# Optimization experiments

Hardware: AMD Instinct MI355X
Metric: run time of the kernel (lower is better)

Reference implementation:

```python
import jax, jax.numpy as jnp
import numpy as np

M = 1024      # mol_dim
H = 1024      # ffn_hidden
T = 2048      # sequence length
NS = 5        # n_solvents
DE = 64       # desc_emb_dim
NB = 3        # ffn/residual blocks
HIN = 2 * M + DE + 1  # beta head input dim


def setup_inputs() -> dict:
    key = jax.random.key(0)
    ks = jax.random.split(key, 32)
    w = lambda i, shape: (0.02 * jax.random.normal(ks[i], shape, dtype=jnp.float32))
    inp = {
        "mol_vec": jax.random.normal(ks[0], (M,), dtype=jnp.float32),
        "solvent_seq": jax.random.uniform(ks[1], (T, NS), dtype=jnp.float32),
        "desc_seq": jax.random.normal(ks[2], (T, 6), dtype=jnp.float32),
        "solvent_vecs": jax.random.normal(ks[3], (NS, M), dtype=jnp.float32),
        "boundary_mask": jnp.zeros((T,), dtype=bool),
        # SolventProjection: Linear(5*M -> M) + 3 residual FFN blocks
        "sp_proj_w": w(4, (NS * M, M)), "sp_proj_b": jnp.zeros((M,), jnp.float32),
        "sp_fc1_w": w(5, (NB, M, M)), "sp_fc1_b": jnp.zeros((NB, M), jnp.float32),
        "sp_fc2_w": w(6, (NB, M, M)), "sp_fc2_b": jnp.zeros((NB, M), jnp.float32),
        "sp_ln_g": jnp.ones((NB, M), jnp.float32), "sp_ln_b": jnp.zeros((NB, M), jnp.float32),
        # desc_proj: Linear(6 -> 64)
        "desc_w": w(7, (6, DE)), "desc_b": jnp.zeros((DE,), jnp.float32),
        "bh_proj_w": w(8, (HIN, H)), "bh_proj_b": jnp.zeros((H,), jnp.float32),
        "bh_fc1_w": w(9, (NB, H, H)), "bh_fc1_b": jnp.zeros((NB, H), jnp.float32),
        "bh_fc2_w": w(10, (NB, H, H)), "bh_fc2_b": jnp.zeros((NB, H), jnp.float32),
        "bh_ln_g": jnp.ones((NB, H), jnp.float32), "bh_ln_b": jnp.zeros((NB, H), jnp.float32),
        "mu_w": w(11, (H,)), "mu_b": jnp.zeros((1,), jnp.float32),
        "phi_w": w(12, (H,)), "phi_b": jnp.zeros((1,), jnp.float32),
    }
    return inp


def _gelu(x):
    return jax.nn.gelu(x, approximate=False)  # torch nn.GELU default (erf)


def _ln(x, g, b, eps=1e-5):
    m = jnp.mean(x, axis=-1, keepdims=True)
    v = jnp.mean((x - m) ** 2, axis=-1, keepdims=True)
    return g * (x - m) * jax.lax.rsqrt(v + eps) + b


def _res_blocks(x, w1, b1, w2, b2, g, b):
    # stack of ResidualFFNBlock (dropout=0 / eval mode)
    for i in range(w1.shape[0]):
        x = _ln(_gelu(x @ w1[i] + b1[i]) @ w2[i] + b2[i] + x, g[i], b[i])
    return x


def reference(mol_vec, solvent_seq, desc_seq, solvent_vecs, boundary_mask,
              sp_proj_w, sp_proj_b, sp_fc1_w, sp_fc1_b, sp_fc2_w, sp_fc2_b, sp_ln_g, sp_ln_b,
              desc_w, desc_b,
              bh_proj_w, bh_proj_b, bh_fc1_w, bh_fc1_b, bh_fc2_w, bh_fc2_b, bh_ln_g, bh_ln_b,
              mu_w, mu_b, phi_w, phi_b):
    def step(prev_rf, xs):
        ratios, desc, is_b = xs  # [5], [6], scalar bool
        # SolventProjection: scale each solvent vec by its ratio, concat, project
        sv = (solvent_vecs * ratios[:, None]).reshape(-1)         # [5*M]
        sp = _gelu(sv @ sp_proj_w + sp_proj_b)                     # [M]
        sp = _res_blocks(sp, sp_fc1_w, sp_fc1_b, sp_fc2_w, sp_fc2_b, sp_ln_g, sp_ln_b)
        demb = _gelu(desc @ desc_w + desc_b)                       # [DE]
        x = jnp.concatenate([mol_vec, sp, demb, prev_rf[None]])   # [HIN]
        z = _gelu(x @ bh_proj_w + bh_proj_b)                       # [H]
        z = _res_blocks(z, bh_fc1_w, bh_fc1_b, bh_fc2_w, bh_fc2_b, bh_ln_g, bh_ln_b)
        mu = jax.nn.sigmoid(jnp.dot(z, mu_w) + mu_b[0])
        phi = jax.nn.softplus(jnp.dot(z, phi_w) + phi_b[0]) + 2.0
        # monotonic update: restart at system boundaries or before first prediction
        rf = jnp.where(is_b | (prev_rf < 0), mu, prev_rf + mu * (1.0 - prev_rf))
        return jax.lax.stop_gradient(rf), (rf, mu, phi)  # prev_rf is detached in torch

    prev0 = jnp.float32(-1.0)
    _, (rfs, mus, phis) = jax.lax.scan(step, prev0, (solvent_seq, desc_seq, boundary_mask))
    return jnp.stack([rfs, mus, phis])  # [3, T]
```

## Files before the change

### kernel.cpp

```cpp
#include <hip/hip_runtime.h>
#include <math.h>

#define MDIM 1024
#define TSEQ 2048
#define NSOL 5
#define DED  64
#define NBLK 3
#define KITER 3
#define XLDB 1088
#define NRED 6144
#define RST  64

typedef __bf16 bf16x8 __attribute__((ext_vector_type(8)));
typedef __bf16 bf16x4 __attribute__((ext_vector_type(4)));
typedef float  f32x4  __attribute__((ext_vector_type(4)));

#define GLDS16(gptr, lptr) __builtin_amdgcn_global_load_lds( \
    (const __attribute__((address_space(1))) unsigned int*)(const void*)(gptr), \
    (__attribute__((address_space(3))) unsigned int*)(void*)(lptr), 16, 0, 0)

__device__ __forceinline__ float gelu_f(float x){
  return 0.5f * x * (1.0f + erff(x * 0.70710678118654752440f));
}
__device__ __forceinline__ float sigmoid_f(float x){ return 1.0f/(1.0f+expf(-x)); }
__device__ __forceinline__ float softplus_f(float x){ return fmaxf(x,0.0f) + log1pf(expf(-fabsf(x))); }

__global__ __launch_bounds__(256) void k_cvtT13(const float* __restrict__ s0,
    const float* __restrict__ s1, const float* __restrict__ s2, const float* __restrict__ s3,
    const float* __restrict__ s4, __bf16* __restrict__ dst, __bf16* __restrict__ WpT){
  __shared__ float t[32][33];
  const size_t MM = (size_t)MDIM*MDIM;
  int z = blockIdx.z;
  int tx = threadIdx.x & 31, ty = threadIdx.x >> 5;
  if (z < 12){
    if (blockIdx.y >= 32) return;
    const float* s = (z<3)? s0 + (size_t)z*MM : (z<6)? s1 + (size_t)(z-3)*MM :
                     (z<9)? s2 + (size_t)(z-6)*MM : s3 + (size_t)(z-9)*MM;
    __bf16* d = dst + (size_t)z*MM;
    int k0 = blockIdx.y*32, n0 = blockIdx.x*32;
    #pragma unroll
    for (int r=0;r<32;r+=8) t[ty+r][tx] = s[(size_t)(k0+ty+r)*MDIM + n0+tx];
    __syncthreads();
    #pragma unroll
    for (int r=0;r<32;r+=8) d[(size_t)(n0+ty+r)*MDIM + k0+tx] = (__bf16)t[tx][ty+r];
  } else {
    int k0 = blockIdx.y*32, n0 = blockIdx.x*32;
    #pragma unroll
    for (int r=0;r<32;r+=8) t[ty+r][tx] = s4[(size_t)(k0+ty+r)*MDIM + n0+tx];
    __syncthreads();
    #pragma unroll
    for (int r=0;r<32;r+=8) WpT[(size_t)(n0+ty+r)*XLDB + k0+tx] = (__bf16)t[tx][ty+r];
  }
}

__global__ __launch_bounds__(256) void k_pm(const float* __restrict__ sv,
    const float* __restrict__ spW, const float* __restrict__ mol,
    const float* __restrict__ bhw, float* __restrict__ PART){
  int s = blockIdx.y;
  int j = blockIdx.x*256 + threadIdx.x;
  int z = blockIdx.z, k0 = z*64;
  if (s < NSOL){
    const float* w = spW + (size_t)s*MDIM*MDIM + (size_t)k0*MDIM + j;
    const float* v = sv + s*MDIM + k0;
    float acc = 0.f;
    for (int k=0;k<64;k++) acc = fmaf(v[k], w[(size_t)k*MDIM], acc);
    PART[(size_t)z*NRED + s*MDIM + j] = acc;
  } else {
    const float* w = bhw + (size_t)k0*MDIM + j;
    float acc = 0.f;
    for (int k=0;k<64;k++) acc = fmaf(mol[k0+k], w[(size_t)k*MDIM], acc);
    PART[(size_t)z*NRED + 5120 + j] = acc;
  }
}

__global__ __launch_bounds__(256) void k_red(const float* __restrict__ PART,
    const float* __restrict__ bhb, float* __restrict__ P, float* __restrict__ mp,
    float* __restrict__ prevg, int* __restrict__ dlist, int* __restrict__ dcnt){
  int i = blockIdx.x*256 + threadIdx.x;
  if (i < TSEQ){ prevg[i] = (i==0)? -1.0f : 1.0f; dlist[i] = i; }
  if (i == 0) *dcnt = TSEQ;
  float a = 0.f;
  #pragma unroll
  for (int z=0;z<16;z++) a += PART[(size_t)z*NRED + i];
  if (i < 5120) P[i] = a;
  else mp[i-5120] = a + bhb[i-5120];
}

__global__ __launch_bounds__(256) void k_sp0d(const float* __restrict__ ratios,
    const float* __restrict__ P, const float* __restrict__ bias,
    const float* __restrict__ desc, const float* __restrict__ dw,
    const float* __restrict__ db,
    float* __restrict__ X, __bf16* __restrict__ Xb){
  int t = blockIdx.y;
  if (blockIdx.x < 4){
    int j = blockIdx.x*256 + threadIdx.x;
    const float* r = ratios + t*NSOL;
    float acc = bias[j];
    #pragma unroll
    for (int s=0;s<NSOL;s++) acc = fmaf(r[s], P[s*MDIM+j], acc);
    float v = gelu_f(acc);
    X[(size_t)t*MDIM + j] = v;
    Xb[(size_t)t*XLDB + j] = (__bf16)v;
  } else if (threadIdx.x < DED){
    int e = threadIdx.x;
    const float* d = desc + t*6;
    float acc = db[e];
    #pragma unroll
    for (int c=0;c<6;c++) acc = fmaf(d[c], dw[c*DED+e], acc);
    Xb[(size_t)t*XLDB + MDIM + e] = (__bf16)gelu_f(acc);
  }
}

template<int BK, bool GELU, bool RES, bool OUTF, bool OUTB, bool Z0>
__global__ __launch_bounds__(512) void k_mfma_gemm(
    const __bf16* __restrict__ A, int lda, int K,
    const __bf16* __restrict__ Bt,
    const float* __restrict__ bias,
    const float* __restrict__ R, int ldr,
    float* __restrict__ Cf, int ldcf,
    __bf16* __restrict__ Cb, int ldcb,
    const float* __restrict__ wlast, const float* __restrict__ prevg,
    float* __restrict__ Z0f, __bf16* __restrict__ Z0b)
{
  constexpr int CPR = BK/8;
  constexpr int AG  = BK/32;
  constexpr int BG  = (BK>=64)? BK/64 : 1;
  constexpr int KS  = BK/32;
  __shared__ __attribute__((aligned(16))) __bf16 As[2][128*BK];
  __shared__ __attribute__((aligned(16))) __bf16 Bs[2][64*BK];
  int tid = threadIdx.x;
  int wave = tid>>6, lane = tid&63;
  int row0 = blockIdx.y*128, col0 = blockIdx.x*64;
  int wr = (wave>>1)*32, wc = (wave&1)*32;
  int lr = lane&15;
  f32x4 acc[2][2] = {};
  int NT = K / BK;

  auto stage = [&](int b, int k0){
    #pragma unroll
    for (int p=0;p<AG;p++){
      int q = wave*(AG*64) + p*64 + lane;
      int r = q/CPR, c = q%CPR, cl = c^(r&7);
      GLDS16(A + (size_t)(row0+r)*lda + k0 + cl*8, &As[b][(wave*(AG*64)+p*64)*8]);
    }
    #pragma unroll
    for (int p=0;p<BG;p++){
      int q = wave*(BG*64) + p*64 + lane;
      int r = q/CPR, c = q%CPR, cl = c^(r&7);
      GLDS16(Bt + (size_t)(col0+r)*K + k0 + cl*8, &Bs[b][(wave*(BG*64)+p*64)*8]);
    }
  };

  stage(0, 0);
  for (int t=0; t<NT; t++){
    __syncthreads();
    if (t+1 < NT) stage((t+1)&1, (t+1)*BK);
    int b = t&1;
    #pragma unroll
    for (int ks=0;ks<KS;ks++){
      int c = ks*4 + (lane>>4);
      bf16x8 af[2], bg[2];
      #pragma unroll
      for (int m=0;m<2;m++){
        int rowA = wr + m*16 + lr;
        af[m] = *(const bf16x8*)&As[b][rowA*BK + ((c ^ (rowA&7))<<3)];
      }
      #pragma unroll
      for (int n=0;n<2;n++){
        int rowB = wc + n*16 + lr;
        bg[n] = *(const bf16x8*)&Bs[b][rowB*BK + ((c ^ (rowB&7))<<3)];
      }
      #pragma unroll
      for (int m=0;m<2;m++)
        #pragma unroll
        for (int n=0;n<2;n++)
          acc[m][n] = __builtin_amdgcn_mfma_f32_16x16x32_bf16(af[m], bg[n], acc[m][n], 0,0,0);
    }
  }
  int rq = (lane>>4)*4;
  #pragma unroll
  for (int m=0;m<2;m++){
    #pragma unroll
    for (int n=0;n<2;n++){
      int cc = col0 + wc + n*16 + lr;
      float bv = bias[cc];
      #pragma unroll
      for (int q=0;q<4;q++){
        int r = row0 + wr + m*16 + rq + q;
        float v = acc[m][n][q] + bv;
        if (RES)  v += R[(size_t)r*ldr + cc];
        if (GELU) v = gelu_f(v);
        if (OUTF) Cf[(size_t)r*ldcf + cc] = v;
        if (OUTB) Cb[(size_t)r*ldcb + cc] = (__bf16)v;
        if (Z0){
          float z = gelu_f(v + prevg[r]*wlast[cc]);
          Z0f[(size_t)r*MDIM + cc] = z;
          Z0b[(size_t)r*MDIM + cc] = (__bf16)z;
        }
      }
    }
  }
}

template<bool MUPHI>
__global__ __launch_bounds__(256) void k_ln(const float* __restrict__ Y, int ldy,
    float* __restrict__ Xo, int ldx, __bf16* __restrict__ Xb, int ldxb,
    const float* __restrict__ g, const float* __restrict__ b,
    const float* __restrict__ muw, const float* __restrict__ mub,
    const float* __restrict__ phiw, const float* __restrict__ phib,
    float* __restrict__ muA, float* __restrict__ phiA)
{
  int t = blockIdx.x;
  __shared__ float red[16];
  int tid = threadIdx.x;
  f32x4 y = *(const f32x4*)&Y[(size_t)t*ldy + tid*4];
  float s  = y[0]+y[1]+y[2]+y[3];
  float s2 = y[0]*y[0]+y[1]*y[1]+y[2]*y[2]+y[3]*y[3];
  for (int o=32;o>0;o>>=1){ s += __shfl_down(s,o); s2 += __shfl_down(s2,o); }
  int wid = tid>>6, lane = tid&63;
  if (lane==0){ red[wid]=s; red[wid+8]=s2; }
  __syncthreads();
  if (tid==0){
    float a=0.f,c=0.f;
    for (int w=0;w<4;w++){ a+=red[w]; c+=red[w+8]; }
    red[0]=a; red[8]=c;
  }
  __syncthreads();
  float mean = red[0]*(1.0f/MDIM);
  float var  = red[8]*(1.0f/MDIM) - mean*mean;
  float rs = rsqrtf(var + 1e-5f);
  f32x4 gv = *(const f32x4*)&g[tid*4];
  f32x4 bb = *(const f32x4*)&b[tid*4];
  f32x4 v; bf16x4 vb;
  #pragma unroll
  for (int i=0;i<4;i++){ v[i] = gv[i]*(y[i]-mean)*rs + bb[i]; vb[i] = (__bf16)v[i]; }
  *(f32x4*)&Xo[(size_t)t*ldx + tid*4] = v;
  *(bf16x4*)&Xb[(size_t)t*ldxb + tid*4] = vb;
  if (MUPHI){
    f32x4 mw = *(const f32x4*)&muw[tid*4];
    f32x4 pw = *(const f32x4*)&phiw[tid*4];
    float sm=0.f, sp=0.f;
    #pragma unroll
    for (int i=0;i<4;i++){ sm = fmaf(v[i], mw[i], sm); sp = fmaf(v[i], pw[i], sp); }
    for (int o=32;o>0;o>>=1){ sm+=__shfl_down(sm,o); sp+=__shfl_down(sp,o); }
    __syncthreads();
    if (lane==0){ red[wid]=sm; red[wid+8]=sp; }
    __syncthreads();
    if (tid==0){
      float a=0.f,c=0.f;
      for (int w=0;w<4;w++){ a+=red[w]; c+=red[w+8]; }
      muA[t]  = sigmoid_f(a + mub[0]);
      phiA[t] = softplus_f(c + phib[0]) + 2.0f;
    }
  }
}


__global__ __launch_bounds__(256) void k_fc1z_dirty(
    const float* __restrict__ ZP, const float* __restrict__ wlast,
    const float* __restrict__ prevg,
    const __bf16* __restrict__ Wt, const float* __restrict__ bias,
    const int* __restrict__ dlist, const int* __restrict__ dcnt,
    float* __restrict__ Z, __bf16* __restrict__ Zb, __bf16* __restrict__ Ob)
{
  __shared__ __bf16 zl[MDIM];
  int nd = *dcnt;
  int jb = blockIdx.x;
  int j = jb*256 + threadIdx.x;
  for (int rs = blockIdx.y; rs < nd; rs += RST){
    int t = dlist[rs];
    float prev = prevg[t];
    #pragma unroll
    for (int q=0;q<4;q++){
      int k = threadIdx.x + 256*q;
      float v = gelu_f(ZP[(size_t)t*MDIM + k] + prev*wlast[k]);
      zl[k] = (__bf16)v;
      if (jb==0){ Z[(size_t)t*MDIM + k] = v; Zb[(size_t)t*MDIM + k] = (__bf16)v; }
    }
    __syncthreads();
    const __bf16* w = Wt + (size_t)j*MDIM;
    float acc = 0.f;
    for (int k=0;k<MDIM;k+=8){
      bf16x8 wv = *(const bf16x8*)&w[k];
      bf16x8 iv = *(const bf16x8*)&zl[k];
      #pragma unroll
      for (int u=0;u<8;u++) acc = fmaf((float)wv[u], (float)iv[u], acc);
    }
    acc = gelu_f(acc + bias[j]);
    Ob[(size_t)t*MDIM + j] = (__bf16)acc;
    __syncthreads();
  }
}

__global__ __launch_bounds__(256) void k_fc2_dirty(
    const __bf16* __restrict__ In, const __bf16* __restrict__ Wt,
    const float* __restrict__ bias, const float* __restrict__ Rz,
    const int* __restrict__ dlist, const int* __restrict__ dcnt,
    float* __restrict__ Of)
{
  int nd = *dcnt;
  int j = blockIdx.x*256 + threadIdx.x;
  for (int rs = blockIdx.y; rs < nd; rs += RST){
    int t = dlist[rs];
    const __bf16* in = In + (size_t)t*MDIM;
    const __bf16* w  = Wt + (size_t)j*MDIM;
    float acc = 0.f;
    for (int k=0;k<MDIM;k+=8){
      bf16x8 wv = *(const bf16x8*)&w[k];
      bf16x8 iv = *(const bf16x8*)&in[k];
      #pragma unroll
      for (int u=0;u<8;u++) acc = fmaf((float)wv[u], (float)iv[u], acc);
    }
    Of[(size_t)t*MDIM + j] = acc + bias[j] + Rz[(size_t)t*MDIM + j];
  }
}

__global__ __launch_bounds__(256) void k_lnfc1_dirty(
    const float* __restrict__ Y,
    const float* __restrict__ g, const float* __restrict__ b,
    const __bf16* __restrict__ Wt, const float* __restrict__ fbias,
    const int* __restrict__ dlist, const int* __restrict__ dcnt,
    float* __restrict__ Z, __bf16* __restrict__ Zb, __bf16* __restrict__ Ob)
{
  __shared__ __bf16 zl[MDIM];
  __shared__ float red[16];
  int nd = *dcnt;
  int jb = blockIdx.x;
  int j = jb*256 + threadIdx.x;
  int wid = threadIdx.x>>6, lane = threadIdx.x&63;
  for (int rs = blockIdx.y; rs < nd; rs += RST){
    int t = dlist[rs];
    float y[4]; float s=0.f, s2=0.f;
    #pragma unroll
    for (int q=0;q<4;q++){
      y[q] = Y[(size_t)t*MDIM + threadIdx.x + 256*q];
      s += y[q]; s2 += y[q]*y[q];
    }
    for (int o=32;o>0;o>>=1){ s += __shfl_down(s,o); s2 += __shfl_down(s2,o); }
    if (lane==0){ red[wid]=s; red[wid+8]=s2; }
    __syncthreads();
    if (threadIdx.x==0){
      float a=0.f,c=0.f;
      for (int w=0;w<4;w++){ a+=red[w]; c+=red[w+8]; }
      red[0]=a; red[8]=c;
    }
    __syncthreads();
    float mean = red[0]*(1.0f/MDIM);
    float var  = red[8]*(1.0f/MDIM) - mean*mean;
    float rs2 = rsqrtf(var + 1e-5f);
    #pragma unroll
    for (int q=0;q<4;q++){
      int k = threadIdx.x + 256*q;
      float v = g[k]*(y[q]-mean)*rs2 + b[k];
      zl[k] = (__bf16)v;
      if (jb==0){ Z[(size_t)t*MDIM + k] = v; Zb[(size_t)t*MDIM + k] = (__bf16)v; }
    }
    __syncthreads();
    const __bf16* w = Wt + (size_t)j*MDIM;
    float acc = 0.f;
    for (int k=0;k<MDIM;k+=8){
      bf16x8 wv = *(const bf16x8*)&w[k];
      bf16x8 iv = *(const bf16x8*)&zl[k];
      #pragma unroll
      for (int u=0;u<8;u++) acc = fmaf((float)wv[u], (float)iv[u], acc);
    }
    acc = gelu_f(acc + fbias[j]);
    Ob[(size_t)t*MDIM + j] = (__bf16)acc;
    __syncthreads();
  }
}

__global__ __launch_bounds__(256) void k_lnmp_dirty(
    const float* __restrict__ Y,
    const float* __restrict__ g, const float* __restrict__ b,
    const int* __restrict__ dlist, const int* __restrict__ dcnt,
    const float* __restrict__ muw, const float* __restrict__ mub,
    const float* __restrict__ phiw, const float* __restrict__ phib,
    float* __restrict__ muA, float* __restrict__ phiA)
{
  int nd = *dcnt;
  __shared__ float red[16];
  int wid = threadIdx.x>>6, lane = threadIdx.x&63;
  for (int rs = blockIdx.x; rs < nd; rs += RST){
    int t = dlist[rs];
    float y[4]; float s=0.f, s2=0.f;
    #pragma unroll
    for (int q=0;q<4;q++){
      y[q] = Y[(size_t)t*MDIM + threadIdx.x + 256*q];
      s += y[q]; s2 += y[q]*y[q];
    }
    for (int o=32;o>0;o>>=1){ s += __shfl_down(s,o); s2 += __shfl_down(s2,o); }
    if (lane==0){ red[wid]=s; red[wid+8]=s2; }
    __syncthreads();
    if (threadIdx.x==0){
      float a=0.f,c=0.f;
      for (int w=0;w<4;w++){ a+=red[w]; c+=red[w+8]; }
      red[0]=a; red[8]=c;
    }
    __syncthreads();
    float mean = red[0]*(1.0f/MDIM);
    float var  = red[8]*(1.0f/MDIM) - mean*mean;
    float rs2 = rsqrtf(var + 1e-5f);
    float sm=0.f, sp=0.f;
    #pragma unroll
    for (int q=0;q<4;q++){
      int k = threadIdx.x + 256*q;
      float v = g[k]*(y[q]-mean)*rs2 + b[k];
      sm = fmaf(v, muw[k], sm); sp = fmaf(v, phiw[k], sp);
    }
    __syncthreads();
    for (int o=32;o>0;o>>=1){ sm+=__shfl_down(sm,o); sp+=__shfl_down(sp,o); }
    if (lane==0){ red[wid]=sm; red[wid+8]=sp; }
    __syncthreads();
    if (threadIdx.x==0){
      float a=0.f,c=0.f;
      for (int w=0;w<4;w++){ a+=red[w]; c+=red[w+8]; }
      muA[t]  = sigmoid_f(a + mub[0]);
      phiA[t] = softplus_f(c + phib[0]) + 2.0f;
    }
    __syncthreads();
  }
}

__global__ __launch_bounds__(1024) void k_scan(
    const float* __restrict__ muA, const float* __restrict__ phiA,
    const unsigned char* __restrict__ bmask,
    float* __restrict__ prevg, int* __restrict__ dlist, int* __restrict__ dcnt,
    float* __restrict__ out)
{
  if (*dcnt == 0) return;
  __shared__ float v[2][TSEQ];
  __shared__ unsigned char f[2][TSEQ];
  __shared__ int cnt;
  int tid = threadIdx.x;
  if (tid==0) cnt = 0;
  for (int i=tid;i<TSEQ;i+=1024){
    v[0][i] = 1.0f - muA[i];
    f[0][i] = (i==0) || (bmask[i] != 0);
  }
  __syncthreads();
  int src=0;
  for (int off=1; off<TSEQ; off<<=1){
    int dst = src^1;
    for (int i=tid;i<TSEQ;i+=1024){
      float vv = v[src][i]; unsigned char ff = f[src][i];
      if (i>=off && !ff){ vv *= v[src][i-off]; ff = f[src][i-off]; }
      v[dst][i]=vv; f[dst][i]=ff;
    }
    __syncthreads();
    src = dst;
  }
  for (int i=tid;i<TSEQ;i+=1024){
    float rf = 1.0f - v[src][i];
    float prev = (i==0) ? -1.0f : (1.0f - v[src][i-1]);
    out[i]        = rf;
    out[TSEQ+i]   = muA[i];
    out[2*TSEQ+i] = phiA[i];
    float old = prevg[i];
    prevg[i] = prev;
    if (fabsf(prev - old) > 1e-3f){
      int pos = atomicAdd(&cnt, 1);
      dlist[pos] = i;
    }
  }
  __syncthreads();
  if (tid==0) *dcnt = cnt;
}

extern "C" void kernel_launch(void* const* d_in, const int* in_sizes, int n_in,
                              void* d_out, int out_size, void* d_ws, size_t ws_size,
                              hipStream_t stream) {
  const float* mol       = (const float*)d_in[0];
  const float* ratios    = (const float*)d_in[1];
  const float* desc      = (const float*)d_in[2];
  const float* svvec     = (const float*)d_in[3];
  const unsigned char* bmask = (const unsigned char*)d_in[4];
  const float* sp_proj_w = (const float*)d_in[5];
  const float* sp_proj_b = (const float*)d_in[6];
  const float* sp_fc1_w  = (const float*)d_in[7];
  const float* sp_fc1_b  = (const float*)d_in[8];
  const float* sp_fc2_w  = (const float*)d_in[9];
  const float* sp_fc2_b  = (const float*)d_in[10];
  const float* sp_ln_g   = (const float*)d_in[11];
  const float* sp_ln_b   = (const float*)d_in[12];
  const float* desc_w    = (const float*)d_in[13];
  const float* desc_b    = (const float*)d_in[14];
  const float* bh_proj_w = (const float*)d_in[15];
  const float* bh_proj_b = (const float*)d_in[16];
  const float* bh_fc1_w  = (const float*)d_in[17];
  const float* bh_fc1_b  = (const float*)d_in[18];
  const float* bh_fc2_w  = (const float*)d_in[19];
  const float* bh_fc2_b  = (const float*)d_in[20];
  const float* bh_ln_g   = (const float*)d_in[21];
  const float* bh_ln_b   = (const float*)d_in[22];
  const float* mu_w      = (const float*)d_in[23];
  const float* mu_b      = (const float*)d_in[24];
  const float* phi_w     = (const float*)d_in[25];
  const float* phi_b     = (const float*)d_in[26];
  float* out = (float*)d_out;

  char* p = (char*)d_ws;
  auto alloc = [&](size_t bytes)->char*{ char* r = p; p += (bytes + 255) & ~(size_t)255; return r; };
  const size_t MM = (size_t)MDIM*MDIM;
  float*  X    = (float*)alloc((size_t)TSEQ*MDIM*4);
  __bf16* Xb   = (__bf16*)alloc((size_t)TSEQ*XLDB*2);
  __bf16* Zb   = (__bf16*)alloc((size_t)TSEQ*MDIM*2);
  float*  Y    = (float*)alloc((size_t)TSEQ*MDIM*4);
  float*  ZP   = (float*)alloc((size_t)TSEQ*MDIM*4);
  __bf16* Hb16 = (__bf16*)alloc((size_t)TSEQ*MDIM*2);
  __bf16* WALL = (__bf16*)alloc(12*MM*2);
  __bf16* WpT  = (__bf16*)alloc((size_t)MDIM*XLDB*2);
  float*  PART = (float*)alloc((size_t)16*NRED*4);
  float*  P    = (float*)alloc((size_t)NSOL*MDIM*4);
  float*  mp   = (float*)alloc(MDIM*4);
  float*  prevg= (float*)alloc(TSEQ*4);
  float*  muA  = (float*)alloc(TSEQ*4);
  float*  phiA = (float*)alloc(TSEQ*4);
  int*    dlist= (int*)alloc(TSEQ*4);
  int*    dcnt = (int*)alloc(256);
  __bf16* W1T = WALL, *W2T = WALL + 3*MM, *U1T = WALL + 6*MM, *U2T = WALL + 9*MM;
  float*  Z    = X;

  k_cvtT13<<<dim3(32,34,13),256,0,stream>>>(sp_fc1_w, sp_fc2_w, bh_fc1_w, bh_fc2_w,
      bh_proj_w + MM, WALL, WpT);
  k_pm<<<dim3(4,6,16),256,0,stream>>>(svvec, sp_proj_w, mol, bh_proj_w, PART);
  k_red<<<dim3(NRED/256),256,0,stream>>>(PART, bh_proj_b, P, mp, prevg, dlist, dcnt);
  k_sp0d<<<dim3(5,TSEQ),256,0,stream>>>(ratios, P, sp_proj_b, desc, desc_w, desc_b, X, Xb);

  const float* wlast = bh_proj_w + (size_t)2112*MDIM;
  for (int i=0;i<NBLK;i++){
    k_mfma_gemm<128,true,false,false,true,false><<<dim3(16,16),512,0,stream>>>(
        Xb, XLDB, MDIM, W1T + i*MM, sp_fc1_b + i*MDIM, nullptr, 0,
        nullptr, 0, Hb16, MDIM, nullptr, nullptr, nullptr, nullptr);
    k_mfma_gemm<128,false,true,true,false,false><<<dim3(16,16),512,0,stream>>>(
        Hb16, MDIM, MDIM, W2T + i*MM, sp_fc2_b + i*MDIM, X, MDIM,
        Y, MDIM, nullptr, 0, nullptr, nullptr, nullptr, nullptr);
    k_ln<false><<<dim3(TSEQ),256,0,stream>>>(Y, MDIM, X, MDIM, Xb, XLDB,
        sp_ln_g + i*MDIM, sp_ln_b + i*MDIM,
        nullptr, nullptr, nullptr, nullptr, nullptr, nullptr);
  }
  k_mfma_gemm<64,false,false,true,false,true><<<dim3(16,16),512,0,stream>>>(
      Xb, XLDB, XLDB, WpT, mp, nullptr, 0, ZP, MDIM, nullptr, 0,
      wlast, prevg, Z, Zb);

  for (int i=0;i<NBLK;i++){
    k_mfma_gemm<128,true,false,false,true,false><<<dim3(16,16),512,0,stream>>>(
        Zb, MDIM, MDIM, U1T + i*MM, bh_fc1_b + i*MDIM, nullptr, 0,
        nullptr, 0, Hb16, MDIM, nullptr, nullptr, nullptr, nullptr);
    k_mfma_gemm<128,false,true,true,false,false><<<dim3(16,16),512,0,stream>>>(
        Hb16, MDIM, MDIM, U2T + i*MM, bh_fc2_b + i*MDIM, Z, MDIM,
        Y, MDIM, nullptr, 0, nullptr, nullptr, nullptr, nullptr);
    if (i < NBLK-1)
      k_ln<false><<<dim3(TSEQ),256,0,stream>>>(Y, MDIM, Z, MDIM, Zb, MDIM,
          bh_ln_g + i*MDIM, bh_ln_b + i*MDIM,
          nullptr, nullptr, nullptr, nullptr, nullptr, nullptr);
    else
      k_ln<true><<<dim3(TSEQ),256,0,stream>>>(Y, MDIM, Z, MDIM, Zb, MDIM,
          bh_ln_g + i*MDIM, bh_ln_b + i*MDIM,
          mu_w, mu_b, phi_w, phi_b, muA, phiA);
  }
  k_scan<<<dim3(1),1024,0,stream>>>(muA, phiA, bmask, prevg, dlist, dcnt, out);

  for (int it=1; it<KITER; it++){
    k_fc1z_dirty<<<dim3(4,RST),256,0,stream>>>(ZP, wlast, prevg,
        U1T, bh_fc1_b, dlist, dcnt, Z, Zb, Hb16);
    k_fc2_dirty<<<dim3(4,RST),256,0,stream>>>(
        Hb16, U2T, bh_fc2_b, Z, dlist, dcnt, Y);
    for (int i=1;i<NBLK;i++){
      k_lnfc1_dirty<<<dim3(4,RST),256,0,stream>>>(Y,
          bh_ln_g + (i-1)*MDIM, bh_ln_b + (i-1)*MDIM,
          U1T + i*MM, bh_fc1_b + i*MDIM, dlist, dcnt, Z, Zb, Hb16);
      k_fc2_dirty<<<dim3(4,RST),256,0,stream>>>(
          Hb16, U2T + i*MM, bh_fc2_b + i*MDIM, Z, dlist, dcnt, Y);
    }
    k_lnmp_dirty<<<dim3(RST),256,0,stream>>>(Y,
        bh_ln_g + (NBLK-1)*MDIM, bh_ln_b + (NBLK-1)*MDIM,
        dlist, dcnt, mu_w, mu_b, phi_w, phi_b, muA, phiA);
    k_scan<<<dim3(1),1024,0,stream>>>(muA, phiA, bmask, prevg, dlist, dcnt, out);
  }
  (void)in_sizes; (void)n_in; (void)out_size; (void)ws_size;
}
```

Measured before the change: 414.7 us.

## Drop fp32 residual copies and shrink dirty kernels to single-wave blocks

```diff
diff --git a/kernel.cpp b/kernel.cpp
--- a/kernel.cpp
+++ b/kernel.cpp
@@ -89,8 +89,7 @@
 __global__ __launch_bounds__(256) void k_sp0d(const float* __restrict__ ratios,
     const float* __restrict__ P, const float* __restrict__ bias,
     const float* __restrict__ desc, const float* __restrict__ dw,
-    const float* __restrict__ db,
-    float* __restrict__ X, __bf16* __restrict__ Xb){
+    const float* __restrict__ db, __bf16* __restrict__ Xb){
   int t = blockIdx.y;
   if (blockIdx.x < 4){
     int j = blockIdx.x*256 + threadIdx.x;
@@ -98,9 +97,7 @@
     float acc = bias[j];
     #pragma unroll
     for (int s=0;s<NSOL;s++) acc = fmaf(r[s], P[s*MDIM+j], acc);
-    float v = gelu_f(acc);
-    X[(size_t)t*MDIM + j] = v;
-    Xb[(size_t)t*XLDB + j] = (__bf16)v;
+    Xb[(size_t)t*XLDB + j] = (__bf16)gelu_f(acc);
   } else if (threadIdx.x < DED){
     int e = threadIdx.x;
     const float* d = desc + t*6;
@@ -116,11 +113,11 @@
     const __bf16* __restrict__ A, int lda, int K,
     const __bf16* __restrict__ Bt,
     const float* __restrict__ bias,
-    const float* __restrict__ R, int ldr,
+    const __bf16* __restrict__ R, int ldr,
     float* __restrict__ Cf, int ldcf,
     __bf16* __restrict__ Cb, int ldcb,
     const float* __restrict__ wlast, const float* __restrict__ prevg,
-    float* __restrict__ Z0f, __bf16* __restrict__ Z0b)
+    __bf16* __restrict__ Z0b)
 {
   constexpr int CPR = BK/8;
   constexpr int AG  = BK/32;
@@ -188,15 +185,11 @@
       for (int q=0;q<4;q++){
         int r = row0 + wr + m*16 + rq + q;
         float v = acc[m][n][q] + bv;
-        if (RES)  v += R[(size_t)r*ldr + cc];
+        if (RES)  v += (float)R[(size_t)r*ldr + cc];
         if (GELU) v = gelu_f(v);
         if (OUTF) Cf[(size_t)r*ldcf + cc] = v;
         if (OUTB) Cb[(size_t)r*ldcb + cc] = (__bf16)v;
-        if (Z0){
-          float z = gelu_f(v + prevg[r]*wlast[cc]);
-          Z0f[(size_t)r*MDIM + cc] = z;
-          Z0b[(size_t)r*MDIM + cc] = (__bf16)z;
-        }
+        if (Z0)   Z0b[(size_t)r*MDIM + cc] = (__bf16)gelu_f(v + prevg[r]*wlast[cc]);
       }
     }
   }
@@ -204,7 +197,7 @@
 
 template<bool MUPHI>
 __global__ __launch_bounds__(256) void k_ln(const float* __restrict__ Y, int ldy,
-    float* __restrict__ Xo, int ldx, __bf16* __restrict__ Xb, int ldxb,
+    __bf16* __restrict__ Xb, int ldxb,
     const float* __restrict__ g, const float* __restrict__ b,
     const float* __restrict__ muw, const float* __restrict__ mub,
     const float* __restrict__ phiw, const float* __restrict__ phib,
@@ -234,7 +227,6 @@
   f32x4 v; bf16x4 vb;
   #pragma unroll
   for (int i=0;i<4;i++){ v[i] = gv[i]*(y[i]-mean)*rs + bb[i]; vb[i] = (__bf16)v[i]; }
-  *(f32x4*)&Xo[(size_t)t*ldx + tid*4] = v;
   *(bf16x4*)&Xb[(size_t)t*ldxb + tid*4] = vb;
   if (MUPHI){
     f32x4 mw = *(const f32x4*)&muw[tid*4];
@@ -256,26 +248,26 @@
 }
 
 
-__global__ __launch_bounds__(256) void k_fc1z_dirty(
+__global__ __launch_bounds__(64) void k_fc1z_dirty(
     const float* __restrict__ ZP, const float* __restrict__ wlast,
     const float* __restrict__ prevg,
     const __bf16* __restrict__ Wt, const float* __restrict__ bias,
     const int* __restrict__ dlist, const int* __restrict__ dcnt,
-    float* __restrict__ Z, __bf16* __restrict__ Zb, __bf16* __restrict__ Ob)
+    __bf16* __restrict__ Zb, __bf16* __restrict__ Ob)
 {
   __shared__ __bf16 zl[MDIM];
   int nd = *dcnt;
   int jb = blockIdx.x;
-  int j = jb*256 + threadIdx.x;
+  int j = jb*64 + threadIdx.x;
   for (int rs = blockIdx.y; rs < nd; rs += RST){
     int t = dlist[rs];
     float prev = prevg[t];
     #pragma unroll
-    for (int q=0;q<4;q++){
-      int k = threadIdx.x + 256*q;
-      float v = gelu_f(ZP[(size_t)t*MDIM + k] + prev*wlast[k]);
-      zl[k] = (__bf16)v;
-      if (jb==0){ Z[(size_t)t*MDIM + k] = v; Zb[(size_t)t*MDIM + k] = (__bf16)v; }
+    for (int q=0;q<16;q++){
+      int k = threadIdx.x + 64*q;
+      __bf16 v = (__bf16)gelu_f(ZP[(size_t)t*MDIM + k] + prev*wlast[k]);
+      zl[k] = v;
+      if (jb==0) Zb[(size_t)t*MDIM + k] = v;
     }
     __syncthreads();
     const __bf16* w = Wt + (size_t)j*MDIM;
@@ -286,20 +278,19 @@
       #pragma unroll
       for (int u=0;u<8;u++) acc = fmaf((float)wv[u], (float)iv[u], acc);
     }
-    acc = gelu_f(acc + bias[j]);
-    Ob[(size_t)t*MDIM + j] = (__bf16)acc;
-    __syncthreads();
-  }
-}
-
-__global__ __launch_bounds__(256) void k_fc2_dirty(
+    Ob[(size_t)t*MDIM + j] = (__bf16)gelu_f(acc + bias[j]);
+    __syncthreads();
+  }
+}
+
+__global__ __launch_bounds__(64) void k_fc2_dirty(
     const __bf16* __restrict__ In, const __bf16* __restrict__ Wt,
-    const float* __restrict__ bias, const float* __restrict__ Rz,
+    const float* __restrict__ bias, const __bf16* __restrict__ Rz,
     const int* __restrict__ dlist, const int* __restrict__ dcnt,
     float* __restrict__ Of)
 {
   int nd = *dcnt;
-  int j = blockIdx.x*256 + threadIdx.x;
+  int j = blockIdx.x*64 + threadIdx.x;
   for (int rs = blockIdx.y; rs < nd; rs += RST){
     int t = dlist[rs];
     const __bf16* in = In + (size_t)t*MDIM;
@@ -311,49 +302,41 @@
       #pragma unroll
       for (int u=0;u<8;u++) acc = fmaf((float)wv[u], (float)iv[u], acc);
     }
-    Of[(size_t)t*MDIM + j] = acc + bias[j] + Rz[(size_t)t*MDIM + j];
-  }
-}
-
-__global__ __launch_bounds__(256) void k_lnfc1_dirty(
+    Of[(size_t)t*MDIM + j] = acc + bias[j] + (float)Rz[(size_t)t*MDIM + j];
+  }
+}
+
+__global__ __launch_bounds__(64) void k_lnfc1_dirty(
     const float* __restrict__ Y,
     const float* __restrict__ g, const float* __restrict__ b,
     const __bf16* __restrict__ Wt, const float* __restrict__ fbias,
     const int* __restrict__ dlist, const int* __restrict__ dcnt,
-    float* __restrict__ Z, __bf16* __restrict__ Zb, __bf16* __restrict__ Ob)
+    __bf16* __restrict__ Zb, __bf16* __restrict__ Ob)
 {
   __shared__ __bf16 zl[MDIM];
-  __shared__ float red[16];
   int nd = *dcnt;
   int jb = blockIdx.x;
-  int j = jb*256 + threadIdx.x;
-  int wid = threadIdx.x>>6, lane = threadIdx.x&63;
+  int j = jb*64 + threadIdx.x;
   for (int rs = blockIdx.y; rs < nd; rs += RST){
     int t = dlist[rs];
-    float y[4]; float s=0.f, s2=0.f;
-    #pragma unroll
-    for (int q=0;q<4;q++){
-      y[q] = Y[(size_t)t*MDIM + threadIdx.x + 256*q];
+    float y[16]; float s=0.f, s2=0.f;
+    #pragma unroll
+    for (int q=0;q<16;q++){
+      y[q] = Y[(size_t)t*MDIM + threadIdx.x + 64*q];
       s += y[q]; s2 += y[q]*y[q];
     }
     for (int o=32;o>0;o>>=1){ s += __shfl_down(s,o); s2 += __shfl_down(s2,o); }
-    if (lane==0){ red[wid]=s; red[wid+8]=s2; }
-    __syncthreads();
-    if (threadIdx.x==0){
-      float a=0.f,c=0.f;
-      for (int w=0;w<4;w++){ a+=red[w]; c+=red[w+8]; }
-      red[0]=a; red[8]=c;
-    }
-    __syncthreads();
-    float mean = red[0]*(1.0f/MDIM);
-    float var  = red[8]*(1.0f/MDIM) - mean*mean;
+    float tot  = __shfl(s, 0);
+    float tot2 = __shfl(s2, 0);
+    float mean = tot*(1.0f/MDIM);
+    float var  = tot2*(1.0f/MDIM) - mean*mean;
     float rs2 = rsqrtf(var + 1e-5f);
     #pragma unroll
-    for (int q=0;q<4;q++){
-      int k = threadIdx.x + 256*q;
-      float v = g[k]*(y[q]-mean)*rs2 + b[k];
-      zl[k] = (__bf16)v;
-      if (jb==0){ Z[(size_t)t*MDIM + k] = v; Zb[(size_t)t*MDIM + k] = (__bf16)v; }
+    for (int q=0;q<16;q++){
+      int k = threadIdx.x + 64*q;
+      __bf16 v = (__bf16)(g[k]*(y[q]-mean)*rs2 + b[k]);
+      zl[k] = v;
+      if (jb==0) Zb[(size_t)t*MDIM + k] = v;
     }
     __syncthreads();
     const __bf16* w = Wt + (size_t)j*MDIM;
@@ -364,13 +347,12 @@
       #pragma unroll
       for (int u=0;u<8;u++) acc = fmaf((float)wv[u], (float)iv[u], acc);
     }
-    acc = gelu_f(acc + fbias[j]);
-    Ob[(size_t)t*MDIM + j] = (__bf16)acc;
-    __syncthreads();
-  }
-}
-
-__global__ __launch_bounds__(256) void k_lnmp_dirty(
+    Ob[(size_t)t*MDIM + j] = (__bf16)gelu_f(acc + fbias[j]);
+    __syncthreads();
+  }
+}
+
+__global__ __launch_bounds__(64) void k_lnmp_dirty(
     const float* __restrict__ Y,
     const float* __restrict__ g, const float* __restrict__ b,
     const int* __restrict__ dlist, const int* __restrict__ dcnt,
@@ -379,46 +361,32 @@
     float* __restrict__ muA, float* __restrict__ phiA)
 {
   int nd = *dcnt;
-  __shared__ float red[16];
-  int wid = threadIdx.x>>6, lane = threadIdx.x&63;
   for (int rs = blockIdx.x; rs < nd; rs += RST){
     int t = dlist[rs];
-    float y[4]; float s=0.f, s2=0.f;
-    #pragma unroll
-    for (int q=0;q<4;q++){
-      y[q] = Y[(size_t)t*MDIM + threadIdx.x + 256*q];
+    float y[16]; float s=0.f, s2=0.f;
+    #pragma unroll
+    for (int q=0;q<16;q++){
+      y[q] = Y[(size_t)t*MDIM + threadIdx.x + 64*q];
       s += y[q]; s2 += y[q]*y[q];
     }
     for (int o=32;o>0;o>>=1){ s += __shfl_down(s,o); s2 += __shfl_down(s2,o); }
-    if (lane==0){ red[wid]=s; red[wid+8]=s2; }
-    __syncthreads();
-    if (threadIdx.x==0){
-      float a=0.f,c=0.f;
-      for (int w=0;w<4;w++){ a+=red[w]; c+=red[w+8]; }
-      red[0]=a; red[8]=c;
-    }
-    __syncthreads();
-    float mean = red[0]*(1.0f/MDIM);
-    float var  = red[8]*(1.0f/MDIM) - mean*mean;
+    float tot  = __shfl(s, 0);
+    float tot2 = __shfl(s2, 0);
+    float mean = tot*(1.0f/MDIM);
+    float var  = tot2*(1.0f/MDIM) - mean*mean;
     float rs2 = rsqrtf(var + 1e-5f);
     float sm=0.f, sp=0.f;
     #pragma unroll
-    for (int q=0;q<4;q++){
-      int k = threadIdx.x + 256*q;
+    for (int q=0;q<16;q++){
+      int k = threadIdx.x + 64*q;
       float v = g[k]*(y[q]-mean)*rs2 + b[k];
       sm = fmaf(v, muw[k], sm); sp = fmaf(v, phiw[k], sp);
     }
-    __syncthreads();
     for (int o=32;o>0;o>>=1){ sm+=__shfl_down(sm,o); sp+=__shfl_down(sp,o); }
-    if (lane==0){ red[wid]=sm; red[wid+8]=sp; }
-    __syncthreads();
     if (threadIdx.x==0){
-      float a=0.f,c=0.f;
-      for (int w=0;w<4;w++){ a+=red[w]; c+=red[w+8]; }
-      muA[t]  = sigmoid_f(a + mub[0]);
-      phiA[t] = softplus_f(c + phib[0]) + 2.0f;
-    }
-    __syncthreads();
+      muA[t]  = sigmoid_f(sm + mub[0]);
+      phiA[t] = softplus_f(sp + phib[0]) + 2.0f;
+    }
   }
 }
 
@@ -502,7 +470,6 @@
   char* p = (char*)d_ws;
   auto alloc = [&](size_t bytes)->char*{ char* r = p; p += (bytes + 255) & ~(size_t)255; return r; };
   const size_t MM = (size_t)MDIM*MDIM;
-  float*  X    = (float*)alloc((size_t)TSEQ*MDIM*4);
   __bf16* Xb   = (__bf16*)alloc((size_t)TSEQ*XLDB*2);
   __bf16* Zb   = (__bf16*)alloc((size_t)TSEQ*MDIM*2);
   float*  Y    = (float*)alloc((size_t)TSEQ*MDIM*4);
@@ -519,61 +486,60 @@
   int*    dlist= (int*)alloc(TSEQ*4);
   int*    dcnt = (int*)alloc(256);
   __bf16* W1T = WALL, *W2T = WALL + 3*MM, *U1T = WALL + 6*MM, *U2T = WALL + 9*MM;
-  float*  Z    = X;
 
   k_cvtT13<<<dim3(32,34,13),256,0,stream>>>(sp_fc1_w, sp_fc2_w, bh_fc1_w, bh_fc2_w,
       bh_proj_w + MM, WALL, WpT);
   k_pm<<<dim3(4,6,16),256,0,stream>>>(svvec, sp_proj_w, mol, bh_proj_w, PART);
   k_red<<<dim3(NRED/256),256,0,stream>>>(PART, bh_proj_b, P, mp, prevg, dlist, dcnt);
-  k_sp0d<<<dim3(5,TSEQ),256,0,stream>>>(ratios, P, sp_proj_b, desc, desc_w, desc_b, X, Xb);
+  k_sp0d<<<dim3(5,TSEQ),256,0,stream>>>(ratios, P, sp_proj_b, desc, desc_w, desc_b, Xb);
 
   const float* wlast = bh_proj_w + (size_t)2112*MDIM;
   for (int i=0;i<NBLK;i++){
     k_mfma_gemm<128,true,false,false,true,false><<<dim3(16,16),512,0,stream>>>(
         Xb, XLDB, MDIM, W1T + i*MM, sp_fc1_b + i*MDIM, nullptr, 0,
-        nullptr, 0, Hb16, MDIM, nullptr, nullptr, nullptr, nullptr);
+        nullptr, 0, Hb16, MDIM, nullptr, nullptr, nullptr);
     k_mfma_gemm<128,false,true,true,false,false><<<dim3(16,16),512,0,stream>>>(
-        Hb16, MDIM, MDIM, W2T + i*MM, sp_fc2_b + i*MDIM, X, MDIM,
-        Y, MDIM, nullptr, 0, nullptr, nullptr, nullptr, nullptr);
-    k_ln<false><<<dim3(TSEQ),256,0,stream>>>(Y, MDIM, X, MDIM, Xb, XLDB,
+        Hb16, MDIM, MDIM, W2T + i*MM, sp_fc2_b + i*MDIM, Xb, XLDB,
+        Y, MDIM, nullptr, 0, nullptr, nullptr, nullptr);
+    k_ln<false><<<dim3(TSEQ),256,0,stream>>>(Y, MDIM, Xb, XLDB,
         sp_ln_g + i*MDIM, sp_ln_b + i*MDIM,
         nullptr, nullptr, nullptr, nullptr, nullptr, nullptr);
   }
   k_mfma_gemm<64,false,false,true,false,true><<<dim3(16,16),512,0,stream>>>(
       Xb, XLDB, XLDB, WpT, mp, nullptr, 0, ZP, MDIM, nullptr, 0,
-      wlast, prevg, Z, Zb);
+      wlast, prevg, Zb);
 
   for (int i=0;i<NBLK;i++){
     k_mfma_gemm<128,true,false,false,true,false><<<dim3(16,16),512,0,stream>>>(
         Zb, MDIM, MDIM, U1T + i*MM, bh_fc1_b + i*MDIM, nullptr, 0,
-        nullptr, 0, Hb16, MDIM, nullptr, nullptr, nullptr, nullptr);
+        nullptr, 0, Hb16, MDIM, nullptr, nullptr, nullptr);
     k_mfma_gemm<128,false,true,true,false,false><<<dim3(16,16),512,0,stream>>>(
-        Hb16, MDIM, MDIM, U2T + i*MM, bh_fc2_b + i*MDIM, Z, MDIM,
-        Y, MDIM, nullptr, 0, nullptr, nullptr, nullptr, nullptr);
+        Hb16, MDIM, MDIM, U2T + i*MM, bh_fc2_b + i*MDIM, Zb, MDIM,
+        Y, MDIM, nullptr, 0, nullptr, nullptr, nullptr);
     if (i < NBLK-1)
-      k_ln<false><<<dim3(TSEQ),256,0,stream>>>(Y, MDIM, Z, MDIM, Zb, MDIM,
+      k_ln<false><<<dim3(TSEQ),256,0,stream>>>(Y, MDIM, Zb, MDIM,
           bh_ln_g + i*MDIM, bh_ln_b + i*MDIM,
           nullptr, nullptr, nullptr, nullptr, nullptr, nullptr);
     else
-      k_ln<true><<<dim3(TSEQ),256,0,stream>>>(Y, MDIM, Z, MDIM, Zb, MDIM,
+      k_ln<true><<<dim3(TSEQ),256,0,stream>>>(Y, MDIM, Zb, MDIM,
           bh_ln_g + i*MDIM, bh_ln_b + i*MDIM,
           mu_w, mu_b, phi_w, phi_b, muA, phiA);
   }
   k_scan<<<dim3(1),1024,0,stream>>>(muA, phiA, bmask, prevg, dlist, dcnt, out);
 
   for (int it=1; it<KITER; it++){
-    k_fc1z_dirty<<<dim3(4,RST),256,0,stream>>>(ZP, wlast, prevg,
-        U1T, bh_fc1_b, dlist, dcnt, Z, Zb, Hb16);
-    k_fc2_dirty<<<dim3(4,RST),256,0,stream>>>(
-        Hb16, U2T, bh_fc2_b, Z, dlist, dcnt, Y);
+    k_fc1z_dirty<<<dim3(16,RST),64,0,stream>>>(ZP, wlast, prevg,
+        U1T, bh_fc1_b, dlist, dcnt, Zb, Hb16);
+    k_fc2_dirty<<<dim3(16,RST),64,0,stream>>>(
+        Hb16, U2T, bh_fc2_b, Zb, dlist, dcnt, Y);
     for (int i=1;i<NBLK;i++){
-      k_lnfc1_dirty<<<dim3(4,RST),256,0,stream>>>(Y,
+      k_lnfc1_dirty<<<dim3(16,RST),64,0,stream>>>(Y,
           bh_ln_g + (i-1)*MDIM, bh_ln_b + (i-1)*MDIM,
-          U1T + i*MM, bh_fc1_b + i*MDIM, dlist, dcnt, Z, Zb, Hb16);
-      k_fc2_dirty<<<dim3(4,RST),256,0,stream>>>(
-          Hb16, U2T + i*MM, bh_fc2_b + i*MDIM, Z, dlist, dcnt, Y);
-    }
-    k_lnmp_dirty<<<dim3(RST),256,0,stream>>>(Y,
+          U1T + i*MM, bh_fc1_b + i*MDIM, dlist, dcnt, Zb, Hb16);
+      k_fc2_dirty<<<dim3(16,RST),64,0,stream>>>(
+          Hb16, U2T + i*MM, bh_fc2_b + i*MDIM, Zb, dlist, dcnt, Y);
+    }
+    k_lnmp_dirty<<<dim3(RST),64,0,stream>>>(Y,
         bh_ln_g + (NBLK-1)*MDIM, bh_ln_b + (NBLK-1)*MDIM,
         dlist, dcnt, mu_w, mu_b, phi_w, phi_b, muA, phiA);
     k_scan<<<dim3(1),1024,0,stream>>>(muA, phiA, bmask, prevg, dlist, dcnt, out);
```

New measurement: 384.4 us. 1.08x faster.
